# Kernel tuning notes

Hardware: AMD Instinct MI355X
Metric: run time of the kernel (lower is better)

The kernel has to match this reference:

```python
import jax, jax.numpy as jnp
import numpy as np

COMPRESS_RATIO = 4
HEAD_DIM = 512
COFF = 2  # overlap (compress_ratio == 4) doubles the projection width
EPS = 1e-6


def setup_inputs() -> dict:
    key = jax.random.key(0)
    k1, k2, k3, k4 = jax.random.split(key, 4)
    B, S, D = 4, 4096, 4096
    OD = COFF * HEAD_DIM  # 1024
    scale = 1.0 / np.sqrt(D)
    return {
        "x": jax.random.normal(k1, (B, S, D), dtype=jnp.float32),
        "wkv_w": jax.random.normal(k2, (OD, D), dtype=jnp.float32) * scale,
        "wgate_w": jax.random.normal(k3, (OD, D), dtype=jnp.float32) * scale,
        "ape": jax.random.normal(k4, (COMPRESS_RATIO, OD), dtype=jnp.float32) * 0.02,
        "norm_w": jnp.ones((HEAD_DIM,), dtype=jnp.float32),
    }


def reference(x, wkv_w, wgate_w, ape, norm_w):
    # x: [B, S, D]; windowed KV compression (NSA-style):
    # gated projection -> per-position learned abs pos embed -> window pool -> RMSNorm
    B, S, D = x.shape
    r = COMPRESS_RATIO
    nW = S // r
    kv = jnp.einsum("bsd,od->bso", x, wkv_w)          # [B, S, coff*hd]
    gate = jax.nn.sigmoid(jnp.einsum("bsd,od->bso", x, wgate_w))
    kv = kv * gate
    # add learned absolute position embedding per position-within-window
    kv = kv + jnp.tile(ape, (nW, 1))                    # [S, coff*hd] broadcast over B
    # pool each window of r tokens; split overlap streams into separate tokens
    kv = kv.reshape(B, nW, r, COFF, HEAD_DIM).mean(axis=2)  # [B, nW, coff, hd]
    kv = kv.reshape(B, nW * COFF, HEAD_DIM)                 # [B, 2*nW, hd]
    # RMSNorm over head_dim
    var = jnp.mean(kv * kv, axis=-1, keepdims=True)
    return norm_w * kv * jax.lax.rsqrt(var + EPS)
```

## Files before the change

kernel.cpp:

```cpp
#include <hip/hip_runtime.h>
#include <hip/hip_bf16.h>

#define D_DIM 4096
#define OD    1024
#define M_TOT 16384
#define N_TOT 2048
#define BM 256
#define BN 256
#define BK 64

#define GLOBAL_AS __attribute__((address_space(1)))
#define LDS_AS    __attribute__((address_space(3)))

typedef __attribute__((ext_vector_type(8))) short          bf16x8;
typedef __attribute__((ext_vector_type(8))) unsigned short u16x8;
typedef __attribute__((ext_vector_type(4))) float          f32x4;

__device__ __forceinline__ unsigned short f2bf(float f) {
    unsigned int u = __float_as_uint(f);
    u = (u + 0x7fffu + ((u >> 16) & 1u)) >> 16;
    return (unsigned short)u;
}

__device__ __forceinline__ float sigm(float x) {
    return 1.0f / (1.0f + __expf(-x));
}

__device__ __forceinline__ void gload16(const void* g, void* l) {
    __builtin_amdgcn_global_load_lds((const GLOBAL_AS void*)g, (LDS_AS void*)l, 16, 0, 0);
}

__global__ void prep_weights(const float* __restrict__ wkv,
                             const float* __restrict__ wgate,
                             unsigned short* __restrict__ Wc) {
    int t  = blockIdx.x * 256 + threadIdx.x;
    int n  = t >> 9;
    int k8 = t & 511;
    const float* src = (n & 1) ? wgate : wkv;
    const float4* s4 = (const float4*)(src + (size_t)(n >> 1) * D_DIM + k8 * 8);
    float4 a = s4[0], b = s4[1];
    u16x8 o;
    o[0] = f2bf(a.x); o[1] = f2bf(a.y); o[2] = f2bf(a.z); o[3] = f2bf(a.w);
    o[4] = f2bf(b.x); o[5] = f2bf(b.y); o[6] = f2bf(b.z); o[7] = f2bf(b.w);
    *(u16x8*)(Wc + (size_t)n * D_DIM + k8 * 8) = o;
}

__global__ void prep_x(const float* __restrict__ x, unsigned short* __restrict__ xb) {
    size_t t = (size_t)blockIdx.x * 256 + threadIdx.x;
    const float4* s = (const float4*)(x + t * 8);
    float4 a = s[0], b = s[1];
    u16x8 o;
    o[0] = f2bf(a.x); o[1] = f2bf(a.y); o[2] = f2bf(a.z); o[3] = f2bf(a.w);
    o[4] = f2bf(b.x); o[5] = f2bf(b.y); o[6] = f2bf(b.z); o[7] = f2bf(b.w);
    *(u16x8*)(xb + t * 8) = o;
}

__global__ void prep_ape(const float* __restrict__ ape, float* __restrict__ am) {
    int t = blockIdx.x * 256 + threadIdx.x;
    if (t < OD)
        am[t] = 0.25f * (ape[t] + ape[OD + t] + ape[2 * OD + t] + ape[3 * OD + t]);
}

extern __shared__ __align__(16) unsigned short smem_u16[];

__global__ __launch_bounds__(512, 2)
void gemm_fused_8ph(const unsigned short* __restrict__ A,
                    const unsigned short* __restrict__ Wc,
                    const float* __restrict__ ape_mean,
                    float* __restrict__ out_pooled) {
    unsigned short* Asb[2] = {smem_u16,               smem_u16 + BM * BK};
    unsigned short* Bsb[2] = {smem_u16 + 2 * BM * BK, smem_u16 + 3 * BM * BK};

    const int tid  = threadIdx.x;
    const int lane = tid & 63;
    const int wave = tid >> 6;
    const int wm   = wave >> 2;
    const int wn   = wave & 3;
    const int h    = lane & 15;
    const int q    = lane >> 4;

    const int bid = blockIdx.x;
    const int j   = bid >> 3;
    const int m0  = ((bid & 7) * 8 + (j >> 3)) * BM;
    const int n0  = (j & 7) * BN;

    const int sc8 = (lane & 7) ^ ((lane >> 3) & 7);
    const unsigned short* Ag = A  + (size_t)(m0 + wave * 8 + (lane >> 3)) * D_DIM + sc8 * 8;
    const unsigned short* Bg = Wc + (size_t)(n0 + (wave & 3) * 8 + (lane >> 3)) * D_DIM + sc8 * 8;
    const int bstripe = wave >> 2;

    const int xorv = (h & 7) << 3;
    const unsigned aoff0 = (unsigned)((wm * 128 + h) * 64);
    const unsigned boff0 = (unsigned)((wn * 64 + h) * 64);
    const unsigned short* aB[2][2];
    const unsigned short* bB[2][2];
#pragma unroll
    for (int b = 0; b < 2; ++b)
#pragma unroll
        for (int ks = 0; ks < 2; ++ks) {
            const unsigned swz = (unsigned)((ks * 32 + q * 8) ^ xorv);
            aB[b][ks] = Asb[b] + aoff0 + swz;
            bB[b][ks] = Bsb[b] + boff0 + swz;
        }

#define STAGE_A(buf, half, kofs)                                                   \
    do {                                                                           \
        gload16(Ag + (size_t)((half) * 64) * D_DIM + (kofs),                       \
                Asb[buf] + ((half) * 64 + wave * 8) * BK);                         \
        gload16(Ag + (size_t)((half) * 64 + 128) * D_DIM + (kofs),                 \
                Asb[buf] + ((half) * 64 + 128 + wave * 8) * BK);                   \
    } while (0)

#define STAGE_B(buf, qb, kofs)                                                     \
    do {                                                                           \
        const int r0_ = (qb) * 32 + bstripe * 64;                                  \
        const int r1_ = (qb) * 32 + (2 + bstripe) * 64;                            \
        gload16(Bg + (size_t)r0_ * D_DIM + (kofs),                                 \
                Bsb[buf] + (r0_ + (wave & 3) * 8) * BK);                           \
        gload16(Bg + (size_t)r1_ * D_DIM + (kofs),                                 \
                Bsb[buf] + (r1_ + (wave & 3) * 8) * BK);                           \
    } while (0)

#define LOAD_A(buf, qa, dst)                                                       \
    do {                                                                           \
        _Pragma("unroll")                                                          \
        for (int mi = 0; mi < 4; ++mi)                                             \
            _Pragma("unroll")                                                      \
            for (int ks = 0; ks < 2; ++ks)                                         \
                dst[mi][ks] = *(const bf16x8*)(aB[buf][ks] +                       \
                              ((qa) * 4 + mi) * 1024);                             \
    } while (0)

#define LOAD_B(buf, qb, dst)                                                       \
    do {                                                                           \
        _Pragma("unroll")                                                          \
        for (int ni = 0; ni < 2; ++ni)                                             \
            _Pragma("unroll")                                                      \
            for (int ks = 0; ks < 2; ++ks)                                         \
                dst[ni][ks] = *(const bf16x8*)(bB[buf][ks] +                       \
                              ((qb) * 2 + ni) * 1024);                             \
    } while (0)

#define MFMA_Q(qa, qb, asrc, bsrc)                                                 \
    do {                                                                           \
        __builtin_amdgcn_s_setprio(1);                                             \
        _Pragma("unroll")                                                          \
        for (int mi = 0; mi < 4; ++mi)                                             \
            _Pragma("unroll")                                                      \
            for (int ni = 0; ni < 2; ++ni)                                         \
                _Pragma("unroll")                                                  \
                for (int ks = 0; ks < 2; ++ks)                                     \
                    acc[(qa) * 4 + mi][(qb) * 2 + ni] =                            \
                        __builtin_amdgcn_mfma_f32_16x16x32_bf16(                   \
                            asrc[mi][ks], bsrc[ni][ks],                            \
                            acc[(qa) * 4 + mi][(qb) * 2 + ni], 0, 0, 0);           \
        __builtin_amdgcn_s_setprio(0);                                             \
    } while (0)

#define BAR() __builtin_amdgcn_s_barrier()
#define VMW4() asm volatile("s_waitcnt vmcnt(4)" ::: "memory")

    f32x4 acc[8][4];
    const f32x4 z = {0.f, 0.f, 0.f, 0.f};
#pragma unroll
    for (int i = 0; i < 8; ++i)
#pragma unroll
        for (int jj = 0; jj < 4; ++jj) acc[i][jj] = z;

    STAGE_A(0, 0, 0); STAGE_A(0, 1, 0); STAGE_B(0, 0, 0); STAGE_B(0, 1, 0);
    STAGE_A(1, 0, 64); STAGE_B(1, 1, 64);
    VMW4();
    BAR();

    for (int kt2 = 0; kt2 < D_DIM; kt2 += 2 * BK) {
        const int kb1 = kt2 + BK;
        const int kna = (kt2 + 2 * BK) & 4095;
        const int knb = (kt2 + 3 * BK) & 4095;
        bf16x8 av[4][2], bv[2][2];

        LOAD_A(0, 0, av); LOAD_B(0, 0, bv);
        STAGE_A(1, 1, kb1); STAGE_B(1, 0, kb1);
        MFMA_Q(0, 0, av, bv);
        LOAD_B(0, 1, bv);
        MFMA_Q(0, 1, av, bv);
        BAR();
        LOAD_A(0, 1, av);
        MFMA_Q(1, 1, av, bv);
        LOAD_B(0, 0, bv);
        STAGE_A(0, 0, kna); STAGE_B(0, 1, kna);
        MFMA_Q(1, 0, av, bv);
        VMW4();
        BAR();
        LOAD_A(1, 0, av); LOAD_B(1, 0, bv);
        STAGE_A(0, 1, kna); STAGE_B(0, 0, kna);
        MFMA_Q(0, 0, av, bv);
        LOAD_B(1, 1, bv);
        MFMA_Q(0, 1, av, bv);
        BAR();
        LOAD_A(1, 1, av);
        MFMA_Q(1, 1, av, bv);
        LOAD_B(1, 0, bv);
        STAGE_A(1, 0, knb); STAGE_B(1, 1, knb);
        MFMA_Q(1, 0, av, bv);
        VMW4();
        BAR();
    }
#undef STAGE_A
#undef STAGE_B
#undef LOAD_A
#undef LOAD_B
#undef MFMA_Q
#undef BAR
#undef VMW4

    const bool is_kv = ((h & 1) == 0);
#pragma unroll
    for (int mi = 0; mi < 8; ++mi) {
        const int mbase = m0 + wm * 128 + mi * 16 + q * 4;
        const int wglob = mbase >> 2;
#pragma unroll
        for (int ni = 0; ni < 4; ++ni) {
            f32x4 kv = acc[mi][ni];
            float g0 = __shfl_xor(kv[0], 1);
            float g1 = __shfl_xor(kv[1], 1);
            float g2 = __shfl_xor(kv[2], 1);
            float g3 = __shfl_xor(kv[3], 1);
            if (is_kv) {
                float s = kv[0] * sigm(g0) + kv[1] * sigm(g1) +
                          kv[2] * sigm(g2) + kv[3] * sigm(g3);
                int n = n0 + wn * 64 + ni * 16 + h;
                int o = n >> 1;
                out_pooled[(size_t)wglob * OD + o] = 0.25f * s + ape_mean[o];
            }
        }
    }
}

__global__ __launch_bounds__(256)
void gemm_fused_f32(const float* __restrict__ Aptr,
                    const unsigned short* __restrict__ Wc,
                    const float* __restrict__ ape_mean,
                    float* __restrict__ out_pooled) {
    __shared__ __align__(16) unsigned short As[128 * BK];
    __shared__ __align__(16) unsigned short Bs[128 * BK];
    const int tid  = threadIdx.x;
    const int lane = tid & 63;
    const int wave = tid >> 6;
    const int wr   = wave >> 1;
    const int wc   = wave & 1;
    const int n0   = blockIdx.x * 128;
    const int m0   = blockIdx.y * 128;
    const int h    = lane & 15;
    const int q    = lane >> 4;

    f32x4 acc[4][4];
    const f32x4 z = {0.f, 0.f, 0.f, 0.f};
#pragma unroll
    for (int i = 0; i < 4; ++i)
#pragma unroll
        for (int jj = 0; jj < 4; ++jj) acc[i][jj] = z;

    for (int kt = 0; kt < D_DIM; kt += BK) {
#pragma unroll
        for (int i = 0; i < 4; ++i) {
            int chunk = tid + i * 256;
            int row = chunk >> 3, c8 = chunk & 7;
            int dst = (row * BK + c8 * 8) ^ ((row & 7) << 3);
            const float4* s = (const float4*)(Aptr + (size_t)(m0 + row) * D_DIM + kt + c8 * 8);
            float4 a = s[0], b = s[1];
            u16x8 o;
            o[0] = f2bf(a.x); o[1] = f2bf(a.y); o[2] = f2bf(a.z); o[3] = f2bf(a.w);
            o[4] = f2bf(b.x); o[5] = f2bf(b.y); o[6] = f2bf(b.z); o[7] = f2bf(b.w);
            *(u16x8*)&As[dst] = o;
        }
#pragma unroll
        for (int i = 0; i < 4; ++i) {
            int chunk = tid + i * 256;
            int row = chunk >> 3, c8 = chunk & 7;
            int dst = (row * BK + c8 * 8) ^ ((row & 7) << 3);
            *(u16x8*)&Bs[dst] =
                *(const u16x8*)(Wc + (size_t)(n0 + row) * D_DIM + kt + c8 * 8);
        }
        __syncthreads();
#pragma unroll
        for (int ks = 0; ks < 2; ++ks) {
            const int kb = ks * 32 + q * 8;
            bf16x8 af[4], bfr[4];
#pragma unroll
            for (int am = 0; am < 4; ++am) {
                int row = wr * 64 + am * 16 + h;
                af[am] = *(const bf16x8*)&As[(row * BK + kb) ^ ((row & 7) << 3)];
            }
#pragma unroll
            for (int bn = 0; bn < 4; ++bn) {
                int row = wc * 64 + bn * 16 + h;
                bfr[bn] = *(const bf16x8*)&Bs[(row * BK + kb) ^ ((row & 7) << 3)];
            }
#pragma unroll
            for (int am = 0; am < 4; ++am)
#pragma unroll
                for (int bn = 0; bn < 4; ++bn)
                    acc[am][bn] = __builtin_amdgcn_mfma_f32_16x16x32_bf16(
                        af[am], bfr[bn], acc[am][bn], 0, 0, 0);
        }
        __syncthreads();
    }
    const bool is_kv = ((h & 1) == 0);
#pragma unroll
    for (int am = 0; am < 4; ++am) {
        const int mbase = m0 + wr * 64 + am * 16 + q * 4;
        const int wglob = mbase >> 2;
#pragma unroll
        for (int bn = 0; bn < 4; ++bn) {
            f32x4 kv = acc[am][bn];
            float g0 = __shfl_xor(kv[0], 1);
            float g1 = __shfl_xor(kv[1], 1);
            float g2 = __shfl_xor(kv[2], 1);
            float g3 = __shfl_xor(kv[3], 1);
            if (is_kv) {
                float s = kv[0] * sigm(g0) + kv[1] * sigm(g1) +
                          kv[2] * sigm(g2) + kv[3] * sigm(g3);
                int n = n0 + wc * 64 + bn * 16 + h;
                int o = n >> 1;
                out_pooled[(size_t)wglob * OD + o] = 0.25f * s + ape_mean[o];
            }
        }
    }
}

__global__ void rmsnorm_inplace(float* __restrict__ out, const float* __restrict__ nw) {
    int token = blockIdx.x * 4 + (threadIdx.x >> 6);
    int lane  = threadIdx.x & 63;
    float4* p = (float4*)(out + (size_t)token * 512);
    float4 v0 = p[lane * 2], v1 = p[lane * 2 + 1];
    float ss = v0.x * v0.x + v0.y * v0.y + v0.z * v0.z + v0.w * v0.w +
               v1.x * v1.x + v1.y * v1.y + v1.z * v1.z + v1.w * v1.w;
#pragma unroll
    for (int off = 32; off > 0; off >>= 1) ss += __shfl_xor(ss, off);
    float rs = rsqrtf(ss * (1.0f / 512.0f) + 1e-6f);
    const float4* w4 = (const float4*)nw;
    float4 w0 = w4[lane * 2], w1 = w4[lane * 2 + 1];
    float4 r0, r1;
    r0.x = v0.x * rs * w0.x; r0.y = v0.y * rs * w0.y;
    r0.z = v0.z * rs * w0.z; r0.w = v0.w * rs * w0.w;
    r1.x = v1.x * rs * w1.x; r1.y = v1.y * rs * w1.y;
    r1.z = v1.z * rs * w1.z; r1.w = v1.w * rs * w1.w;
    p[lane * 2]     = r0;
    p[lane * 2 + 1] = r1;
}

extern "C" void kernel_launch(void* const* d_in, const int* in_sizes, int n_in,
                              void* d_out, int out_size, void* d_ws, size_t ws_size,
                              hipStream_t stream) {
    const float* x     = (const float*)d_in[0];
    const float* wkv   = (const float*)d_in[1];
    const float* wgate = (const float*)d_in[2];
    const float* ape   = (const float*)d_in[3];
    const float* normw = (const float*)d_in[4];
    float* out = (float*)d_out;

    unsigned short* Wc  = (unsigned short*)d_ws;
    float* ape_mean     = (float*)((char*)d_ws + (size_t)16 * 1024 * 1024);
    unsigned short* xb  = (unsigned short*)((char*)d_ws + (size_t)16 * 1024 * 1024 + 65536);
    const size_t need_xb = (size_t)16 * 1024 * 1024 + 65536 + (size_t)M_TOT * D_DIM * 2;
    const bool use_xb = (ws_size >= need_xb);

    prep_weights<<<4096, 256, 0, stream>>>(wkv, wgate, Wc);
    prep_ape<<<4, 256, 0, stream>>>(ape, ape_mean);

    if (use_xb) {
        prep_x<<<32768, 256, 0, stream>>>(x, xb);
        (void)hipFuncSetAttribute(
            reinterpret_cast<const void*>(&gemm_fused_8ph),
            hipFuncAttributeMaxDynamicSharedMemorySize, 131072);
        gemm_fused_8ph<<<(M_TOT / BM) * (N_TOT / BN), 512, 131072, stream>>>(
            xb, Wc, ape_mean, out);
    } else {
        gemm_fused_f32<<<dim3(N_TOT / 128, M_TOT / 128), 256, 0, stream>>>(
            x, Wc, ape_mean, out);
    }

    rmsnorm_inplace<<<2048, 256, 0, stream>>>(out, normw);
}
```

Measured before the change: 303.5 us.

## Fuse fp32-to-bf16 conversion of x into the GEMM A-tile staging

Removes the separate prep_x pass and the bf16 copy of x. The GEMM now loads fp32 x into registers, converts it to bf16 and writes it to LDS itself, restaged within the 8-phase pipeline using explicit vmcnt and lgkmcnt waits. This saves one full read and write of the activation through HBM. In exchange, each A tile pulls twice as many bytes into the GEMM, conversion ALU work lands in the main loop, and register pressure rises at 2 blocks per CU. The fp32 fallback kernel and the workspace-size branch are deleted.

```diff
diff --git a/kernel.cpp b/kernel.cpp
--- a/kernel.cpp
+++ b/kernel.cpp
@@ -45,16 +45,6 @@
     *(u16x8*)(Wc + (size_t)n * D_DIM + k8 * 8) = o;
 }
 
-__global__ void prep_x(const float* __restrict__ x, unsigned short* __restrict__ xb) {
-    size_t t = (size_t)blockIdx.x * 256 + threadIdx.x;
-    const float4* s = (const float4*)(x + t * 8);
-    float4 a = s[0], b = s[1];
-    u16x8 o;
-    o[0] = f2bf(a.x); o[1] = f2bf(a.y); o[2] = f2bf(a.z); o[3] = f2bf(a.w);
-    o[4] = f2bf(b.x); o[5] = f2bf(b.y); o[6] = f2bf(b.z); o[7] = f2bf(b.w);
-    *(u16x8*)(xb + t * 8) = o;
-}
-
 __global__ void prep_ape(const float* __restrict__ ape, float* __restrict__ am) {
     int t = blockIdx.x * 256 + threadIdx.x;
     if (t < OD)
@@ -63,8 +53,10 @@
 
 extern __shared__ __align__(16) unsigned short smem_u16[];
 
+struct AFrag { float4 v0, v1, v2, v3; };
+
 __global__ __launch_bounds__(512, 2)
-void gemm_fused_8ph(const unsigned short* __restrict__ A,
+void gemm_fused_8ph(const float* __restrict__ X,
                     const unsigned short* __restrict__ Wc,
                     const float* __restrict__ ape_mean,
                     float* __restrict__ out_pooled) {
@@ -85,7 +77,7 @@
     const int n0  = (j & 7) * BN;
 
     const int sc8 = (lane & 7) ^ ((lane >> 3) & 7);
-    const unsigned short* Ag = A  + (size_t)(m0 + wave * 8 + (lane >> 3)) * D_DIM + sc8 * 8;
+    const float*          Af = X  + (size_t)(m0 + wave * 8 + (lane >> 3)) * D_DIM + sc8 * 8;
     const unsigned short* Bg = Wc + (size_t)(n0 + (wave & 3) * 8 + (lane >> 3)) * D_DIM + sc8 * 8;
     const int bstripe = wave >> 2;
 
@@ -103,12 +95,32 @@
             bB[b][ks] = Bsb[b] + boff0 + swz;
         }
 
-#define STAGE_A(buf, half, kofs)                                                   \
-    do {                                                                           \
-        gload16(Ag + (size_t)((half) * 64) * D_DIM + (kofs),                       \
-                Asb[buf] + ((half) * 64 + wave * 8) * BK);                         \
-        gload16(Ag + (size_t)((half) * 64 + 128) * D_DIM + (kofs),                 \
-                Asb[buf] + ((half) * 64 + 128 + wave * 8) * BK);                   \
+    unsigned short* AsW0 = Asb[0] + (wave * 8) * BK + lane * 8;
+    unsigned short* AsW1 = Asb[1] + (wave * 8) * BK + lane * 8;
+
+#define AISSUE(frag, kofs, half)                                                   \
+    do {                                                                           \
+        const float* p0_ = Af + (size_t)((half) * 64) * D_DIM + (kofs);            \
+        frag.v0 = *(const float4*)(p0_);                                           \
+        frag.v1 = *(const float4*)(p0_ + 4);                                       \
+        frag.v2 = *(const float4*)(p0_ + (size_t)128 * D_DIM);                     \
+        frag.v3 = *(const float4*)(p0_ + (size_t)128 * D_DIM + 4);                 \
+    } while (0)
+
+#define AWRITE(buf, half, frag)                                                    \
+    do {                                                                           \
+        u16x8 w0_, w1_;                                                            \
+        w0_[0] = f2bf(frag.v0.x); w0_[1] = f2bf(frag.v0.y);                        \
+        w0_[2] = f2bf(frag.v0.z); w0_[3] = f2bf(frag.v0.w);                        \
+        w0_[4] = f2bf(frag.v1.x); w0_[5] = f2bf(frag.v1.y);                        \
+        w0_[6] = f2bf(frag.v1.z); w0_[7] = f2bf(frag.v1.w);                        \
+        w1_[0] = f2bf(frag.v2.x); w1_[1] = f2bf(frag.v2.y);                        \
+        w1_[2] = f2bf(frag.v2.z); w1_[3] = f2bf(frag.v2.w);                        \
+        w1_[4] = f2bf(frag.v3.x); w1_[5] = f2bf(frag.v3.y);                        \
+        w1_[6] = f2bf(frag.v3.z); w1_[7] = f2bf(frag.v3.w);                        \
+        unsigned short* d_ = ((buf) ? AsW1 : AsW0) + (half) * 64 * BK;             \
+        *(u16x8*)(d_)             = w0_;                                           \
+        *(u16x8*)(d_ + 128 * BK)  = w1_;                                           \
     } while (0)
 
 #define STAGE_B(buf, qb, kofs)                                                     \
@@ -157,8 +169,9 @@
         __builtin_amdgcn_s_setprio(0);                                             \
     } while (0)
 
-#define BAR() __builtin_amdgcn_s_barrier()
-#define VMW4() asm volatile("s_waitcnt vmcnt(4)" ::: "memory")
+#define BAR()   __builtin_amdgcn_s_barrier()
+#define VMW(n)  asm volatile("s_waitcnt vmcnt(" #n ")" ::: "memory")
+#define LGKM0() asm volatile("s_waitcnt lgkmcnt(0)" ::: "memory")
 
     f32x4 acc[8][4];
     const f32x4 z = {0.f, 0.f, 0.f, 0.f};
@@ -167,51 +180,69 @@
 #pragma unroll
         for (int jj = 0; jj < 4; ++jj) acc[i][jj] = z;
 
-    STAGE_A(0, 0, 0); STAGE_A(0, 1, 0); STAGE_B(0, 0, 0); STAGE_B(0, 1, 0);
-    STAGE_A(1, 0, 64); STAGE_B(1, 1, 64);
-    VMW4();
+    AFrag fa, fb;
+
+    AISSUE(fa, 0, 0);
+    VMW(0);
+    AWRITE(0, 0, fa);
+    STAGE_B(0, 0, 0); STAGE_B(0, 1, 0);
+    AISSUE(fb, 0, 1);
+    VMW(4);
+    LGKM0();
     BAR();
 
     for (int kt2 = 0; kt2 < D_DIM; kt2 += 2 * BK) {
         const int kb1 = kt2 + BK;
         const int kna = (kt2 + 2 * BK) & 4095;
-        const int knb = (kt2 + 3 * BK) & 4095;
         bf16x8 av[4][2], bv[2][2];
 
         LOAD_A(0, 0, av); LOAD_B(0, 0, bv);
-        STAGE_A(1, 1, kb1); STAGE_B(1, 0, kb1);
+        AISSUE(fa, kb1, 0);
+        STAGE_B(1, 0, kb1); STAGE_B(1, 1, kb1);
+        VMW(8);
+        AWRITE(0, 1, fb);
         MFMA_Q(0, 0, av, bv);
         LOAD_B(0, 1, bv);
         MFMA_Q(0, 1, av, bv);
-        BAR();
+        LGKM0(); BAR();
+
         LOAD_A(0, 1, av);
+        AISSUE(fb, kb1, 1);
+        VMW(4);
+        AWRITE(1, 0, fa);
         MFMA_Q(1, 1, av, bv);
         LOAD_B(0, 0, bv);
-        STAGE_A(0, 0, kna); STAGE_B(0, 1, kna);
         MFMA_Q(1, 0, av, bv);
-        VMW4();
-        BAR();
+        LGKM0(); BAR();
+
         LOAD_A(1, 0, av); LOAD_B(1, 0, bv);
-        STAGE_A(0, 1, kna); STAGE_B(0, 0, kna);
+        AISSUE(fa, kna, 0);
+        STAGE_B(0, 0, kna); STAGE_B(0, 1, kna);
+        VMW(8);
+        AWRITE(1, 1, fb);
         MFMA_Q(0, 0, av, bv);
         LOAD_B(1, 1, bv);
         MFMA_Q(0, 1, av, bv);
-        BAR();
+        LGKM0(); BAR();
+
         LOAD_A(1, 1, av);
+        AISSUE(fb, kna, 1);
+        VMW(4);
+        AWRITE(0, 0, fa);
         MFMA_Q(1, 1, av, bv);
         LOAD_B(1, 0, bv);
-        STAGE_A(1, 0, knb); STAGE_B(1, 1, knb);
         MFMA_Q(1, 0, av, bv);
-        VMW4();
-        BAR();
+        LGKM0(); BAR();
     }
-#undef STAGE_A
+#undef AISSUE
+#undef AWRITE
 #undef STAGE_B
 #undef LOAD_A
 #undef LOAD_B
 #undef MFMA_Q
 #undef BAR
-#undef VMW4
+#undef VMW
+#undef LGKM0
 
     const bool is_kv = ((h & 1) == 0);
 #pragma unroll
@@ -236,98 +267,6 @@
     }
 }
 
-__global__ __launch_bounds__(256)
-void gemm_fused_f32(const float* __restrict__ Aptr,
-                    const unsigned short* __restrict__ Wc,
-                    const float* __restrict__ ape_mean,
-                    float* __restrict__ out_pooled) {
-    __shared__ __align__(16) unsigned short As[128 * BK];
-    __shared__ __align__(16) unsigned short Bs[128 * BK];
-    const int tid  = threadIdx.x;
-    const int lane = tid & 63;
-    const int wave = tid >> 6;
-    const int wr   = wave >> 1;
-    const int wc   = wave & 1;
-    const int n0   = blockIdx.x * 128;
-    const int m0   = blockIdx.y * 128;
-    const int h    = lane & 15;
-    const int q    = lane >> 4;
-
-    f32x4 acc[4][4];
-    const f32x4 z = {0.f, 0.f, 0.f, 0.f};
-#pragma unroll
-    for (int i = 0; i < 4; ++i)
-#pragma unroll
-        for (int jj = 0; jj < 4; ++jj) acc[i][jj] = z;
-
-    for (int kt = 0; kt < D_DIM; kt += BK) {
-#pragma unroll
-        for (int i = 0; i < 4; ++i) {
-            int chunk = tid + i * 256;
-            int row = chunk >> 3, c8 = chunk & 7;
-            int dst = (row * BK + c8 * 8) ^ ((row & 7) << 3);
-            const float4* s = (const float4*)(Aptr + (size_t)(m0 + row) * D_DIM + kt + c8 * 8);
-            float4 a = s[0], b = s[1];
-            u16x8 o;
-            o[0] = f2bf(a.x); o[1] = f2bf(a.y); o[2] = f2bf(a.z); o[3] = f2bf(a.w);
-            o[4] = f2bf(b.x); o[5] = f2bf(b.y); o[6] = f2bf(b.z); o[7] = f2bf(b.w);
-            *(u16x8*)&As[dst] = o;
-        }
-#pragma unroll
-        for (int i = 0; i < 4; ++i) {
-            int chunk = tid + i * 256;
-            int row = chunk >> 3, c8 = chunk & 7;
-            int dst = (row * BK + c8 * 8) ^ ((row & 7) << 3);
-            *(u16x8*)&Bs[dst] =
-                *(const u16x8*)(Wc + (size_t)(n0 + row) * D_DIM + kt + c8 * 8);
-        }
-        __syncthreads();
-#pragma unroll
-        for (int ks = 0; ks < 2; ++ks) {
-            const int kb = ks * 32 + q * 8;
-            bf16x8 af[4], bfr[4];
-#pragma unroll
-            for (int am = 0; am < 4; ++am) {
-                int row = wr * 64 + am * 16 + h;
-                af[am] = *(const bf16x8*)&As[(row * BK + kb) ^ ((row & 7) << 3)];
-            }
-#pragma unroll
-            for (int bn = 0; bn < 4; ++bn) {
-                int row = wc * 64 + bn * 16 + h;
-                bfr[bn] = *(const bf16x8*)&Bs[(row * BK + kb) ^ ((row & 7) << 3)];
-            }
-#pragma unroll
-            for (int am = 0; am < 4; ++am)
-#pragma unroll
-                for (int bn = 0; bn < 4; ++bn)
-                    acc[am][bn] = __builtin_amdgcn_mfma_f32_16x16x32_bf16(
-                        af[am], bfr[bn], acc[am][bn], 0, 0, 0);
-        }
-        __syncthreads();
-    }
-    const bool is_kv = ((h & 1) == 0);
-#pragma unroll
-    for (int am = 0; am < 4; ++am) {
-        const int mbase = m0 + wr * 64 + am * 16 + q * 4;
-        const int wglob = mbase >> 2;
-#pragma unroll
-        for (int bn = 0; bn < 4; ++bn) {
-            f32x4 kv = acc[am][bn];
-            float g0 = __shfl_xor(kv[0], 1);
-            float g1 = __shfl_xor(kv[1], 1);
-            float g2 = __shfl_xor(kv[2], 1);
-            float g3 = __shfl_xor(kv[3], 1);
-            if (is_kv) {
-                float s = kv[0] * sigm(g0) + kv[1] * sigm(g1) +
-                          kv[2] * sigm(g2) + kv[3] * sigm(g3);
-                int n = n0 + wc * 64 + bn * 16 + h;
-                int o = n >> 1;
-                out_pooled[(size_t)wglob * OD + o] = 0.25f * s + ape_mean[o];
-            }
-        }
-    }
-}
-
 __global__ void rmsnorm_inplace(float* __restrict__ out, const float* __restrict__ nw) {
     int token = blockIdx.x * 4 + (threadIdx.x >> 6);
     int lane  = threadIdx.x & 63;
@@ -361,24 +300,15 @@
 
     unsigned short* Wc  = (unsigned short*)d_ws;
     float* ape_mean     = (float*)((char*)d_ws + (size_t)16 * 1024 * 1024);
-    unsigned short* xb  = (unsigned short*)((char*)d_ws + (size_t)16 * 1024 * 1024 + 65536);
-    const size_t need_xb = (size_t)16 * 1024 * 1024 + 65536 + (size_t)M_TOT * D_DIM * 2;
-    const bool use_xb = (ws_size >= need_xb);
 
     prep_weights<<<4096, 256, 0, stream>>>(wkv, wgate, Wc);
     prep_ape<<<4, 256, 0, stream>>>(ape, ape_mean);
 
-    if (use_xb) {
-        prep_x<<<32768, 256, 0, stream>>>(x, xb);
-        (void)hipFuncSetAttribute(
-            reinterpret_cast<const void*>(&gemm_fused_8ph),
-            hipFuncAttributeMaxDynamicSharedMemorySize, 131072);
-        gemm_fused_8ph<<<(M_TOT / BM) * (N_TOT / BN), 512, 131072, stream>>>(
-            xb, Wc, ape_mean, out);
-    } else {
-        gemm_fused_f32<<<dim3(N_TOT / 128, M_TOT / 128), 256, 0, stream>>>(
-            x, Wc, ape_mean, out);
-    }
+    (void)hipFuncSetAttribute(
+        reinterpret_cast<const void*>(&gemm_fused_8ph),
+        hipFuncAttributeMaxDynamicSharedMemorySize, 131072);
+    gemm_fused_8ph<<<(M_TOT / BM) * (N_TOT / BN), 512, 131072, stream>>>(
+        x, Wc, ape_mean, out);
 
     rmsnorm_inplace<<<2048, 256, 0, stream>>>(out, normw);
 }
```

Result: slower. 386.9 us (+27.5%).
